# Performance work log

Measured on AMD Instinct MI355X. Metric: run time of the kernel, lower is better.

The kernel has to match this reference:

```python
import jax, jax.numpy as jnp
import numpy as np

B, S, D, DFF = 4, 2048, 1024, 4096
EPS = 1e-5


def layernorm(x, g, b):
    mu = jnp.mean(x, axis=-1, keepdims=True)
    var = jnp.mean(jnp.square(x - mu), axis=-1, keepdims=True)
    return (x - mu) * jax.lax.rsqrt(var + EPS) * g + b


def setup_inputs() -> dict:
    key = jax.random.key(0)
    ks = jax.random.split(key, 4)
    hidden_state = jax.random.normal(ks[0], (B, S, D), dtype=jnp.float32)
    attention_mask = jnp.zeros((B, 1, S), dtype=jnp.float32)  # additive mask
    w1 = jax.random.normal(ks[1], (D, DFF), dtype=jnp.float32) * (1.0 / np.sqrt(D))
    b1 = jnp.zeros((DFF,), dtype=jnp.float32)
    w2 = jax.random.normal(ks[2], (DFF, D), dtype=jnp.float32) * (1.0 / np.sqrt(DFF))
    b2 = jnp.zeros((D,), dtype=jnp.float32)
    ln1_g = jnp.ones((D,), dtype=jnp.float32)
    ln1_b = jnp.zeros((D,), dtype=jnp.float32)
    ln2_g = jnp.ones((D,), dtype=jnp.float32)
    ln2_b = jnp.zeros((D,), dtype=jnp.float32)
    return dict(hidden_state=hidden_state, attention_mask=attention_mask,
                w1=w1, b1=b1, w2=w2, b2=b2,
                ln1_g=ln1_g, ln1_b=ln1_b, ln2_g=ln2_g, ln2_b=ln2_b)


def reference(hidden_state, attention_mask, w1, b1, w2, b2, ln1_g, ln1_b, ln2_g, ln2_b):
    x = hidden_state
    d = jnp.asarray(x.shape[-1], x.dtype)
    # hand-rolled single-head attention: q=k=v=x (source forward ignores QKV projections)
    scores = jnp.einsum('bqd,bkd->bqk', x, x) / jnp.sqrt(d) + attention_mask  # [B,S,S]
    attn = jax.nn.softmax(scores, axis=-1)
    attn_out = jnp.einsum('bqk,bkd->bqd', attn, x)
    h = layernorm(x + attn_out, ln1_g, ln1_b)
    # FFN: dense -> exact GELU -> linear_2
    ffn = jnp.einsum('bsf,fd->bsd', jax.nn.gelu(jnp.einsum('bsd,df->bsf', h, w1) + b1, approximate=False), w2) + b2
    return layernorm(h + ffn, ln2_g, ln2_b)
```

## Files before the change

kernel.cpp:

```cpp
#include <hip/hip_runtime.h>
#include <hip/hip_bf16.h>
#include <math.h>

#define LN_EPS 1e-5f

typedef short short8 __attribute__((ext_vector_type(8)));
typedef float floatx4 __attribute__((ext_vector_type(4)));

__device__ inline unsigned short f2bf(float f) {
    unsigned int u = __float_as_uint(f);
    u += 0x7fff + ((u >> 16) & 1);
    return (unsigned short)(u >> 16);
}

__device__ inline void gl_lds16(const unsigned short* g, unsigned short* l) {
    __builtin_amdgcn_global_load_lds(
        (__attribute__((address_space(1))) const void*)g,
        (__attribute__((address_space(3))) void*)l, 16, 0, 0);
}

__device__ inline float gelu_f(float v) {
    float u2 = 2.0f * v * (0.7978845608f + 0.0356774081f * v * v);
    float t  = 1.0f - 2.0f / (__expf(u2) + 1.0f);
    return 0.5f * v * (1.0f + t);
}

template<int EPI>
__global__ __launch_bounds__(256) void gemm_bt(
    const unsigned short* __restrict__ A, const unsigned short* __restrict__ B,
    const float* __restrict__ bias, void* __restrict__ Cptr,
    int M, int N, int K, long sA, long sB, long sC, long sBias, float scale)
{
    __shared__ unsigned short lds_a[2 * 128 * 32];
    __shared__ unsigned short lds_b[2 * 128 * 32];

    const int tid  = threadIdx.x;
    const int lane = tid & 63;
    const int wave = tid >> 6;
    const int quad = lane >> 4;
    const int l16  = lane & 15;
    const int wm = wave >> 1, wn = wave & 1;
    const int tile_m = blockIdx.y * 128;
    const int tile_n = blockIdx.x * 128;
    const int batch  = blockIdx.z;

    const unsigned short* Ab = A + (size_t)batch * sA;
    const unsigned short* Bb = B + (size_t)batch * sB;

    const int srow = wave * 16 + (lane >> 2);
    const int scol = (lane & 3) * 8;
    const unsigned short* gA0 = Ab + (size_t)(tile_m + srow) * K + scol;
    const unsigned short* gA1 = Ab + (size_t)(tile_m + 64 + srow) * K + scol;
    const unsigned short* gB0 = Bb + (size_t)(tile_n + srow) * K + scol;
    const unsigned short* gB1 = Bb + (size_t)(tile_n + 64 + srow) * K + scol;
    unsigned short* lA0 = &lds_a[wave * 512 + lane * 8];
    unsigned short* lA1 = &lds_a[2048 + wave * 512 + lane * 8];
    unsigned short* lB0 = &lds_b[wave * 512 + lane * 8];
    unsigned short* lB1 = &lds_b[2048 + wave * 512 + lane * 8];

    floatx4 acc[4][4];
    const floatx4 zero = {0.f, 0.f, 0.f, 0.f};
#pragma unroll
    for (int i = 0; i < 4; i++)
#pragma unroll
        for (int j = 0; j < 4; j++) acc[i][j] = zero;

    for (int k0 = 0; k0 < K; k0 += 64) {
        __syncthreads();
        gl_lds16(gA0 + k0, lA0);
        gl_lds16(gA1 + k0, lA1);
        gl_lds16(gB0 + k0, lB0);
        gl_lds16(gB1 + k0, lB1);
        gl_lds16(gA0 + k0 + 32, lA0 + 4096);
        gl_lds16(gA1 + k0 + 32, lA1 + 4096);
        gl_lds16(gB0 + k0 + 32, lB0 + 4096);
        gl_lds16(gB1 + k0 + 32, lB1 + 4096);
        __syncthreads();

#pragma unroll
        for (int h = 0; h < 2; h++) {
            short8 afr[4], bfr[4];
#pragma unroll
            for (int i = 0; i < 4; i++)
                afr[i] = *(const short8*)
                    &lds_a[h * 4096 + (wm * 64 + i * 16 + l16) * 32 + quad * 8];
#pragma unroll
            for (int j = 0; j < 4; j++)
                bfr[j] = *(const short8*)
                    &lds_b[h * 4096 + (wn * 64 + j * 16 + l16) * 32 + quad * 8];
#pragma unroll
            for (int i = 0; i < 4; i++)
#pragma unroll
                for (int j = 0; j < 4; j++)
                    acc[i][j] = __builtin_amdgcn_mfma_f32_16x16x32_bf16(
                        afr[i], bfr[j], acc[i][j], 0, 0, 0);
        }
    }

#pragma unroll
    for (int i = 0; i < 4; i++) {
#pragma unroll
        for (int j = 0; j < 4; j++) {
            int col = tile_n + wn * 64 + j * 16 + l16;
            float addv = 0.f;
            if (EPI == 1 || EPI == 2) addv = bias[col];
            if (EPI == 3) addv = bias[(size_t)batch * sBias + col];
#pragma unroll
            for (int r = 0; r < 4; r++) {
                int row = tile_m + wm * 64 + i * 16 + quad * 4 + r;
                float v = acc[i][j][r];
                if (EPI == 3) v = v * scale + addv;
                else if (EPI >= 1) v += addv;
                if (EPI == 2) v = gelu_f(v);
                if (EPI == 2 || EPI == 3) {
                    unsigned short* C = (unsigned short*)Cptr + (size_t)batch * sC;
                    C[(size_t)row * N + col] = f2bf(v);
                } else {
                    float* C = (float*)Cptr + (size_t)batch * sC;
                    C[(size_t)row * N + col] = v;
                }
            }
        }
    }
}

__global__ __launch_bounds__(256) void cvt_bf16_kernel(
    const float* __restrict__ in, unsigned short* __restrict__ out)
{
    size_t i = ((size_t)blockIdx.x * 256 + threadIdx.x) * 4;
    float4 v = *(const float4*)(in + i);
    ushort4 h;
    h.x = f2bf(v.x); h.y = f2bf(v.y); h.z = f2bf(v.z); h.w = f2bf(v.w);
    *(ushort4*)(out + i) = h;
}

__global__ __launch_bounds__(256) void transpose_cvt_kernel(
    const float* __restrict__ in, unsigned short* __restrict__ out,
    int R, int C, long sIn, long sOut)
{
    __shared__ float tile[32][33];
    const int tc = blockIdx.x * 32, tr = blockIdx.y * 32;
    const float* src = in + (size_t)blockIdx.z * sIn;
    unsigned short* dst = out + (size_t)blockIdx.z * sOut;
    const int tx = threadIdx.x & 31, ty = threadIdx.x >> 5;
#pragma unroll
    for (int i = 0; i < 4; i++)
        tile[ty + i * 8][tx] = src[(size_t)(tr + ty + i * 8) * C + tc + tx];
    __syncthreads();
#pragma unroll
    for (int i = 0; i < 4; i++)
        dst[(size_t)(tc + ty + i * 8) * R + tr + tx] = f2bf(tile[tx][ty + i * 8]);
}

__global__ __launch_bounds__(256) void softmax_bf16_kernel(
    const unsigned short* __restrict__ scores, unsigned short* __restrict__ probs,
    int S)
{
    __shared__ float red[4];
    const int row = blockIdx.x;
    const unsigned short* p = scores + (size_t)row * S;
    unsigned short* pr      = probs  + (size_t)row * S;
    const int tid  = threadIdx.x;
    const int lane = tid & 63;
    const int wav  = tid >> 6;

    uint4 raw = *(const uint4*)(p + tid * 8);
    float v[8];
    v[0] = __uint_as_float(raw.x << 16); v[1] = __uint_as_float(raw.x & 0xffff0000u);
    v[2] = __uint_as_float(raw.y << 16); v[3] = __uint_as_float(raw.y & 0xffff0000u);
    v[4] = __uint_as_float(raw.z << 16); v[5] = __uint_as_float(raw.z & 0xffff0000u);
    v[6] = __uint_as_float(raw.w << 16); v[7] = __uint_as_float(raw.w & 0xffff0000u);

    float mx = v[0];
#pragma unroll
    for (int k = 1; k < 8; k++) mx = fmaxf(mx, v[k]);
#pragma unroll
    for (int off = 32; off > 0; off >>= 1) mx = fmaxf(mx, __shfl_down(mx, off));
    if (lane == 0) red[wav] = mx;
    __syncthreads();
    mx = fmaxf(fmaxf(red[0], red[1]), fmaxf(red[2], red[3]));
    __syncthreads();

    float s = 0.f;
#pragma unroll
    for (int k = 0; k < 8; k++) { v[k] = __expf(v[k] - mx); s += v[k]; }
#pragma unroll
    for (int off = 32; off > 0; off >>= 1) s += __shfl_down(s, off);
    if (lane == 0) red[wav] = s;
    __syncthreads();
    s = red[0] + red[1] + red[2] + red[3];
    float inv = 1.0f / s;

    uint4 o;
    o.x = (unsigned)f2bf(v[0] * inv) | ((unsigned)f2bf(v[1] * inv) << 16);
    o.y = (unsigned)f2bf(v[2] * inv) | ((unsigned)f2bf(v[3] * inv) << 16);
    o.z = (unsigned)f2bf(v[4] * inv) | ((unsigned)f2bf(v[5] * inv) << 16);
    o.w = (unsigned)f2bf(v[6] * inv) | ((unsigned)f2bf(v[7] * inv) << 16);
    *(uint4*)(pr + tid * 8) = o;
}

template<int WRITE_BF16>
__global__ __launch_bounds__(256) void add_ln_kernel(
    const float* __restrict__ X, const float* __restrict__ Y,
    const float* __restrict__ g, const float* __restrict__ bta,
    float* __restrict__ out, unsigned short* __restrict__ out16, int D)
{
    __shared__ float red[8];
    const int row = blockIdx.x;
    const float* x = X + (size_t)row * D;
    const float* y = Y + (size_t)row * D;
    const int tid  = threadIdx.x;
    const int lane = tid & 63;
    const int wav  = tid >> 6;

    float4 a  = *(const float4*)(x + tid * 4);
    float4 b4 = *(const float4*)(y + tid * 4);
    float v0 = a.x + b4.x, v1 = a.y + b4.y, v2 = a.z + b4.z, v3 = a.w + b4.w;

    float s1 = v0 + v1 + v2 + v3;
    float s2 = v0 * v0 + v1 * v1 + v2 * v2 + v3 * v3;
#pragma unroll
    for (int off = 32; off > 0; off >>= 1) {
        s1 += __shfl_down(s1, off);
        s2 += __shfl_down(s2, off);
    }
    if (lane == 0) { red[wav] = s1; red[4 + wav] = s2; }
    __syncthreads();
    s1 = red[0] + red[1] + red[2] + red[3];
    s2 = red[4] + red[5] + red[6] + red[7];
    const float mu  = s1 / (float)D;
    const float var = s2 / (float)D - mu * mu;
    const float rs  = rsqrtf(var + LN_EPS);

    float4 gg = *(const float4*)(g + tid * 4);
    float4 bb = *(const float4*)(bta + tid * 4);
    float4 r;
    r.x = (v0 - mu) * rs * gg.x + bb.x;
    r.y = (v1 - mu) * rs * gg.y + bb.y;
    r.z = (v2 - mu) * rs * gg.z + bb.z;
    r.w = (v3 - mu) * rs * gg.w + bb.w;
    *(float4*)(out + (size_t)row * D + tid * 4) = r;
    if (WRITE_BF16) {
        ushort4 h;
        h.x = f2bf(r.x); h.y = f2bf(r.y); h.z = f2bf(r.z); h.w = f2bf(r.w);
        *(ushort4*)(out16 + (size_t)row * D + tid * 4) = h;
    }
}

extern "C" void kernel_launch(void* const* d_in, const int* in_sizes, int n_in,
                              void* d_out, int out_size, void* d_ws, size_t ws_size,
                              hipStream_t stream) {
    (void)in_sizes; (void)n_in; (void)out_size; (void)ws_size;
    const float* x    = (const float*)d_in[0];
    const float* mask = (const float*)d_in[1];
    const float* w1   = (const float*)d_in[2];
    const float* b1   = (const float*)d_in[3];
    const float* w2   = (const float*)d_in[4];
    const float* b2   = (const float*)d_in[5];
    const float* ln1g = (const float*)d_in[6];
    const float* ln1b = (const float*)d_in[7];
    const float* ln2g = (const float*)d_in[8];
    const float* ln2b = (const float*)d_in[9];
    float* out = (float*)d_out;

    const int B = 4, S = 2048, D = 1024, DFF = 4096;

    char* ws = (char*)d_ws;
    unsigned short* scoresb = (unsigned short*)ws;
    unsigned short* act     = (unsigned short*)ws;
    char* r1 = ws + (size_t)64 * 1024 * 1024;
    unsigned short* xb    = (unsigned short*)r1;
    unsigned short* probs = (unsigned short*)r1;
    unsigned short* hb16  = (unsigned short*)r1;
    float*          ffn   = (float*)r1;
    float* hbuf = (float*)(ws + (size_t)96 * 1024 * 1024);
    unsigned short* xTb = (unsigned short*)d_out;
    unsigned short* w1T = (unsigned short*)((char*)d_out + (size_t)16 * 1024 * 1024);
    unsigned short* w2T = (unsigned short*)((char*)d_out + (size_t)24 * 1024 * 1024);

    cvt_bf16_kernel<<<(B * S * D) / 1024, 256, 0, stream>>>(x, xb);
    transpose_cvt_kernel<<<dim3(D / 32, S / 32, B), 256, 0, stream>>>(
        x, xTb, S, D, (long)S * D, (long)S * D);
    transpose_cvt_kernel<<<dim3(DFF / 32, D / 32, 1), 256, 0, stream>>>(
        w1, w1T, D, DFF, 0L, 0L);
    transpose_cvt_kernel<<<dim3(D / 32, DFF / 32, 1), 256, 0, stream>>>(
        w2, w2T, DFF, D, 0L, 0L);

    hipLaunchKernelGGL((gemm_bt<3>), dim3(S / 128, S / 128, B), dim3(256), 0, stream,
                       xb, xb, mask, (void*)scoresb,
                       S, S, D, (long)S * D, (long)S * D, (long)S * S, (long)S, 0.03125f);
    softmax_bf16_kernel<<<B * S, 256, 0, stream>>>(scoresb, probs, S);
    hipLaunchKernelGGL((gemm_bt<0>), dim3(D / 128, S / 128, B), dim3(256), 0, stream,
                       probs, xTb, (const float*)nullptr, (void*)hbuf,
                       S, D, S, (long)S * S, (long)D * S, (long)S * D, 0L, 0.f);
    hipLaunchKernelGGL((add_ln_kernel<1>), dim3(B * S), dim3(256), 0, stream,
                       x, hbuf, ln1g, ln1b, hbuf, hb16, D);
    hipLaunchKernelGGL((gemm_bt<2>), dim3(DFF / 128, (B * S) / 128, 1), dim3(256), 0, stream,
                       hb16, w1T, b1, (void*)act,
                       B * S, DFF, D, 0L, 0L, 0L, 0L, 0.f);
    hipLaunchKernelGGL((gemm_bt<1>), dim3(D / 128, (B * S) / 128, 1), dim3(256), 0, stream,
                       act, w2T, b2, (void*)ffn,
                       B * S, D, DFF, 0L, 0L, 0L, 0L, 0.f);
    hipLaunchKernelGGL((add_ln_kernel<0>), dim3(B * S), dim3(256), 0, stream,
                       hbuf, ffn, ln2g, ln2b, out, (unsigned short*)nullptr, D);
}
```

Before: 473.1 us.

## Fuse residual adds into GEMM epilogues, vectorize stores, merge x conversion kernels

Swaps the MFMA operand order so each lane holds four consecutive columns, which lets the GEMM epilogue load bias and residual and store results as 4-wide vectors instead of scalar strided stores. The residual additions before both layernorms move into the attention-output and FFN2 GEMM epilogues, so the layernorm kernels read one tensor instead of two. The straight and transposed bf16 conversions of x are merged into a single pass, and the workspace layout is rearranged to fit. This cuts memory traffic and kernel launches, at the cost of reading the residual inside the GEMMs and reusing d_out as scratch for the FFN sum.

```diff
diff --git a/kernel.cpp b/kernel.cpp
--- a/kernel.cpp
+++ b/kernel.cpp
@@ -28,7 +28,8 @@
 template<int EPI>
 __global__ __launch_bounds__(256) void gemm_bt(
     const unsigned short* __restrict__ A, const unsigned short* __restrict__ B,
-    const float* __restrict__ bias, void* __restrict__ Cptr,
+    const float* __restrict__ bias, const float* __restrict__ resid,
+    void* __restrict__ Cptr,
     int M, int N, int K, long sA, long sB, long sC, long sBias, float scale)
 {
     __shared__ unsigned short lds_a[2 * 128 * 32];
@@ -93,63 +94,89 @@
 #pragma unroll
                 for (int j = 0; j < 4; j++)
                     acc[i][j] = __builtin_amdgcn_mfma_f32_16x16x32_bf16(
-                        afr[i], bfr[j], acc[i][j], 0, 0, 0);
+                        bfr[j], afr[i], acc[i][j], 0, 0, 0);
         }
     }
 
 #pragma unroll
     for (int i = 0; i < 4; i++) {
+        const int row = tile_m + wm * 64 + i * 16 + l16;
 #pragma unroll
         for (int j = 0; j < 4; j++) {
-            int col = tile_n + wn * 64 + j * 16 + l16;
-            float addv = 0.f;
-            if (EPI == 1 || EPI == 2) addv = bias[col];
-            if (EPI == 3) addv = bias[(size_t)batch * sBias + col];
-#pragma unroll
-            for (int r = 0; r < 4; r++) {
-                int row = tile_m + wm * 64 + i * 16 + quad * 4 + r;
-                float v = acc[i][j][r];
-                if (EPI == 3) v = v * scale + addv;
-                else if (EPI >= 1) v += addv;
-                if (EPI == 2) v = gelu_f(v);
-                if (EPI == 2 || EPI == 3) {
-                    unsigned short* C = (unsigned short*)Cptr + (size_t)batch * sC;
-                    C[(size_t)row * N + col] = f2bf(v);
-                } else {
-                    float* C = (float*)Cptr + (size_t)batch * sC;
-                    C[(size_t)row * N + col] = v;
-                }
+            const int colb = tile_n + wn * 64 + j * 16 + quad * 4;
+            float v[4];
+#pragma unroll
+            for (int r = 0; r < 4; r++) v[r] = acc[i][j][r];
+
+            if (EPI == 3) {
+                float4 mv = *(const float4*)&bias[(size_t)batch * sBias + colb];
+                v[0] = v[0] * scale + mv.x;  v[1] = v[1] * scale + mv.y;
+                v[2] = v[2] * scale + mv.z;  v[3] = v[3] * scale + mv.w;
+            }
+            if (EPI == 2 || EPI == 5) {
+                float4 bv = *(const float4*)&bias[colb];
+                v[0] += bv.x; v[1] += bv.y; v[2] += bv.z; v[3] += bv.w;
+            }
+            if (EPI == 2) {
+#pragma unroll
+                for (int r = 0; r < 4; r++) v[r] = gelu_f(v[r]);
+            }
+            if (EPI == 4 || EPI == 5) {
+                float4 rv = *(const float4*)&resid[(size_t)batch * sC +
+                                                   (size_t)row * N + colb];
+                v[0] += rv.x; v[1] += rv.y; v[2] += rv.z; v[3] += rv.w;
+            }
+
+            if (EPI == 2 || EPI == 3) {
+                unsigned short* C = (unsigned short*)Cptr + (size_t)batch * sC;
+                ushort4 h4;
+                h4.x = f2bf(v[0]); h4.y = f2bf(v[1]);
+                h4.z = f2bf(v[2]); h4.w = f2bf(v[3]);
+                *(ushort4*)(C + (size_t)row * N + colb) = h4;
+            } else {
+                float* C = (float*)Cptr + (size_t)batch * sC;
+                float4 f4 = {v[0], v[1], v[2], v[3]};
+                *(float4*)(C + (size_t)row * N + colb) = f4;
             }
         }
     }
 }
 
-__global__ __launch_bounds__(256) void cvt_bf16_kernel(
-    const float* __restrict__ in, unsigned short* __restrict__ out)
-{
-    size_t i = ((size_t)blockIdx.x * 256 + threadIdx.x) * 4;
-    float4 v = *(const float4*)(in + i);
-    ushort4 h;
-    h.x = f2bf(v.x); h.y = f2bf(v.y); h.z = f2bf(v.z); h.w = f2bf(v.w);
-    *(ushort4*)(out + i) = h;
-}
-
-__global__ __launch_bounds__(256) void transpose_cvt_kernel(
-    const float* __restrict__ in, unsigned short* __restrict__ out,
-    int R, int C, long sIn, long sOut)
+__global__ __launch_bounds__(256) void x_prep_kernel(
+    const float* __restrict__ in, unsigned short* __restrict__ straight,
+    unsigned short* __restrict__ transposed, int R, int C, long sIn)
 {
     __shared__ float tile[32][33];
     const int tc = blockIdx.x * 32, tr = blockIdx.y * 32;
     const float* src = in + (size_t)blockIdx.z * sIn;
-    unsigned short* dst = out + (size_t)blockIdx.z * sOut;
+    unsigned short* dstS = straight   + (size_t)blockIdx.z * sIn;
+    unsigned short* dstT = transposed + (size_t)blockIdx.z * sIn;
     const int tx = threadIdx.x & 31, ty = threadIdx.x >> 5;
 #pragma unroll
+    for (int i = 0; i < 4; i++) {
+        float val = src[(size_t)(tr + ty + i * 8) * C + tc + tx];
+        tile[ty + i * 8][tx] = val;
+        dstS[(size_t)(tr + ty + i * 8) * C + tc + tx] = f2bf(val);
+    }
+    __syncthreads();
+#pragma unroll
     for (int i = 0; i < 4; i++)
-        tile[ty + i * 8][tx] = src[(size_t)(tr + ty + i * 8) * C + tc + tx];
-    __syncthreads();
+        dstT[(size_t)(tc + ty + i * 8) * R + tr + tx] = f2bf(tile[tx][ty + i * 8]);
+}
+
+__global__ __launch_bounds__(256) void transpose_cvt_kernel(
+    const float* __restrict__ in, unsigned short* __restrict__ out, int R, int C)
+{
+    __shared__ float tile[32][33];
+    const int tc = blockIdx.x * 32, tr = blockIdx.y * 32;
+    const int tx = threadIdx.x & 31, ty = threadIdx.x >> 5;
 #pragma unroll
     for (int i = 0; i < 4; i++)
-        dst[(size_t)(tc + ty + i * 8) * R + tr + tx] = f2bf(tile[tx][ty + i * 8]);
+        tile[ty + i * 8][tx] = in[(size_t)(tr + ty + i * 8) * C + tc + tx];
+    __syncthreads();
+#pragma unroll
+    for (int i = 0; i < 4; i++)
+        out[(size_t)(tc + ty + i * 8) * R + tr + tx] = f2bf(tile[tx][ty + i * 8]);
 }
 
 __global__ __launch_bounds__(256) void softmax_bf16_kernel(
@@ -200,22 +227,20 @@
 }
 
 template<int WRITE_BF16>
-__global__ __launch_bounds__(256) void add_ln_kernel(
-    const float* __restrict__ X, const float* __restrict__ Y,
+__global__ __launch_bounds__(256) void ln_kernel(
+    const float* __restrict__ X,
     const float* __restrict__ g, const float* __restrict__ bta,
     float* __restrict__ out, unsigned short* __restrict__ out16, int D)
 {
     __shared__ float red[8];
     const int row = blockIdx.x;
     const float* x = X + (size_t)row * D;
-    const float* y = Y + (size_t)row * D;
     const int tid  = threadIdx.x;
     const int lane = tid & 63;
     const int wav  = tid >> 6;
 
-    float4 a  = *(const float4*)(x + tid * 4);
-    float4 b4 = *(const float4*)(y + tid * 4);
-    float v0 = a.x + b4.x, v1 = a.y + b4.y, v2 = a.z + b4.z, v3 = a.w + b4.w;
+    float4 a = *(const float4*)(x + tid * 4);
+    float v0 = a.x, v1 = a.y, v2 = a.z, v3 = a.w;
 
     float s1 = v0 + v1 + v2 + v3;
     float s2 = v0 * v0 + v1 * v1 + v2 * v2 + v3 * v3;
@@ -264,43 +289,40 @@
     float* out = (float*)d_out;
 
     const int B = 4, S = 2048, D = 1024, DFF = 4096;
+    const size_t MB = 1024 * 1024;
 
     char* ws = (char*)d_ws;
     unsigned short* scoresb = (unsigned short*)ws;
     unsigned short* act     = (unsigned short*)ws;
-    char* r1 = ws + (size_t)64 * 1024 * 1024;
-    unsigned short* xb    = (unsigned short*)r1;
-    unsigned short* probs = (unsigned short*)r1;
-    unsigned short* hb16  = (unsigned short*)r1;
-    float*          ffn   = (float*)r1;
-    float* hbuf = (float*)(ws + (size_t)96 * 1024 * 1024);
-    unsigned short* xTb = (unsigned short*)d_out;
-    unsigned short* w1T = (unsigned short*)((char*)d_out + (size_t)16 * 1024 * 1024);
-    unsigned short* w2T = (unsigned short*)((char*)d_out + (size_t)24 * 1024 * 1024);
-
-    cvt_bf16_kernel<<<(B * S * D) / 1024, 256, 0, stream>>>(x, xb);
-    transpose_cvt_kernel<<<dim3(D / 32, S / 32, B), 256, 0, stream>>>(
-        x, xTb, S, D, (long)S * D, (long)S * D);
-    transpose_cvt_kernel<<<dim3(DFF / 32, D / 32, 1), 256, 0, stream>>>(
-        w1, w1T, D, DFF, 0L, 0L);
-    transpose_cvt_kernel<<<dim3(D / 32, DFF / 32, 1), 256, 0, stream>>>(
-        w2, w2T, DFF, D, 0L, 0L);
+    unsigned short* xb      = (unsigned short*)(ws + 32 * MB);
+    unsigned short* probs   = (unsigned short*)(ws + 32 * MB);
+    float*          hbuf    = (float*)(ws + 64 * MB);
+    unsigned short* hb16    = (unsigned short*)(ws + 96 * MB);
+    unsigned short* w1T     = (unsigned short*)(ws + 112 * MB);
+    unsigned short* w2T     = (unsigned short*)(ws + 120 * MB);
+    unsigned short* xTb     = (unsigned short*)d_out;
+    float*          fsum    = (float*)d_out;
+
+    x_prep_kernel<<<dim3(D / 32, S / 32, B), 256, 0, stream>>>(
+        x, xb, xTb, S, D, (long)S * D);
+    transpose_cvt_kernel<<<dim3(DFF / 32, D / 32, 1), 256, 0, stream>>>(w1, w1T, D, DFF);
+    transpose_cvt_kernel<<<dim3(D / 32, DFF / 32, 1), 256, 0, stream>>>(w2, w2T, DFF, D);
 
     hipLaunchKernelGGL((gemm_bt<3>), dim3(S / 128, S / 128, B), dim3(256), 0, stream,
-                       xb, xb, mask, (void*)scoresb,
+                       xb, xb, mask, (const float*)nullptr, (void*)scoresb,
                        S, S, D, (long)S * D, (long)S * D, (long)S * S, (long)S, 0.03125f);
     softmax_bf16_kernel<<<B * S, 256, 0, stream>>>(scoresb, probs, S);
-    hipLaunchKernelGGL((gemm_bt<0>), dim3(D / 128, S / 128, B), dim3(256), 0, stream,
-                       probs, xTb, (const float*)nullptr, (void*)hbuf,
+    hipLaunchKernelGGL((gemm_bt<4>), dim3(D / 128, S / 128, B), dim3(256), 0, stream,
+                       probs, xTb, (const float*)nullptr, x, (void*)hbuf,
                        S, D, S, (long)S * S, (long)D * S, (long)S * D, 0L, 0.f);
-    hipLaunchKernelGGL((add_ln_kernel<1>), dim3(B * S), dim3(256), 0, stream,
-                       x, hbuf, ln1g, ln1b, hbuf, hb16, D);
+    hipLaunchKernelGGL((ln_kernel<1>), dim3(B * S), dim3(256), 0, stream,
+                       hbuf, ln1g, ln1b, hbuf, hb16, D);
     hipLaunchKernelGGL((gemm_bt<2>), dim3(DFF / 128, (B * S) / 128, 1), dim3(256), 0, stream,
-                       hb16, w1T, b1, (void*)act,
+                       hb16, w1T, b1, (const float*)nullptr, (void*)act,
                        B * S, DFF, D, 0L, 0L, 0L, 0L, 0.f);
-    hipLaunchKernelGGL((gemm_bt<1>), dim3(D / 128, (B * S) / 128, 1), dim3(256), 0, stream,
-                       act, w2T, b2, (void*)ffn,
+    hipLaunchKernelGGL((gemm_bt<5>), dim3(D / 128, (B * S) / 128, 1), dim3(256), 0, stream,
+                       act, w2T, b2, hbuf, (void*)fsum,
                        B * S, D, DFF, 0L, 0L, 0L, 0L, 0.f);
-    hipLaunchKernelGGL((add_ln_kernel<0>), dim3(B * S), dim3(256), 0, stream,
-                       hbuf, ffn, ln2g, ln2b, out, (unsigned short*)nullptr, D);
-}
+    hipLaunchKernelGGL((ln_kernel<0>), dim3(B * S), dim3(256), 0, stream,
+                       fsum, ln2g, ln2b, out, (unsigned short*)nullptr, D);
+}
```

Result: no change. 477.2 us (+0.9%).
